# Performance work log

Measured on AMD Instinct MI355X. Metric: run time of the kernel, lower is better.

Reference implementation:

```python
import jax, jax.numpy as jnp
import numpy as np

# ---- module constants (from init_kwargs) ----
VOXEL_SIZE = np.array([0.1, 0.1, 0.2], np.float32)
PC_RANGE = np.array([0.0, -40.0, -3.0, 70.4, 40.0, 1.0], np.float32)
MAX_PTS = 10            # max_points_in_voxel
MAX_VOX = 40000         # max_voxel_num (hard voxelization cap per sample)
GRID = np.round((PC_RANGE[3:] - PC_RANGE[:3]) / VOXEL_SIZE).astype(np.int32)  # [704,800,20] (x,y,z)
BIG = int(GRID[0]) * int(GRID[1]) * int(GRID[2])

PC_MIN = jnp.asarray(PC_RANGE[:3])
VSIZE = jnp.asarray(VOXEL_SIZE)
GRID_J = jnp.asarray(GRID)

B = 8
N_PER_B = 120000


def setup_inputs() -> dict:
    key = jax.random.key(0)
    k1, = jax.random.split(key, 1)
    u = jax.random.uniform(k1, (B * N_PER_B, 4), dtype=jnp.float32)
    # place points inside (and slightly around) pc_range
    x = u[:, 0] * 72.0 - 0.5
    y = u[:, 1] * 82.0 - 41.0
    z = u[:, 2] * 4.4 - 3.2
    inten = u[:, 3]
    bs_idx = jnp.repeat(jnp.arange(B, dtype=jnp.float32), N_PER_B)
    points = jnp.stack([bs_idx, x, y, z, inten], axis=1)  # [960000, 5]
    return {"points": points, "batch_size": B}


def _voxelize_one(pts):
    """Hard voxelization of one point cloud pts [N,4] -> fixed-size buffers.
    Faithful to first-come voxel ordering and per-voxel point caps."""
    N = pts.shape[0]
    idxs = jnp.arange(N, dtype=jnp.int32)
    xyz = pts[:, :3]
    c = jnp.floor((xyz - PC_MIN) / VSIZE).astype(jnp.int32)  # [N,3] (x,y,z)
    valid = jnp.all((c >= 0) & (c < GRID_J), axis=1)
    lid = (c[:, 2] * GRID[1] + c[:, 1]) * GRID[0] + c[:, 0]  # z-major linear id
    lid = jnp.where(valid, lid, BIG)

    order = jnp.argsort(lid)            # stable: within a voxel, original order kept
    lid_s = lid[order]
    is_new = jnp.concatenate([jnp.ones((1,), bool), lid_s[1:] != lid_s[:-1]])
    gid = jnp.cumsum(is_new.astype(jnp.int32)) - 1           # group id per sorted point
    starts = jax.lax.cummax(jnp.where(is_new, idxs, 0))      # group start position
    pos = idxs - starts                                      # rank inside its voxel

    g_lid = jax.ops.segment_min(lid_s, gid, num_segments=N)
    g_valid = g_lid < BIG
    first_orig = jax.ops.segment_min(order.astype(jnp.int32), gid, num_segments=N)
    # voxel slot = first-appearance rank (invalid/empty groups pushed to the end)
    first_key = jnp.where(g_valid, first_orig, N + idxs)
    perm = jnp.argsort(first_key)
    slot = jnp.zeros(N, jnp.int32).at[perm].set(idxs)

    pslot = slot[gid]
    keep = g_valid[gid] & (pslot < MAX_VOX) & (pos < MAX_PTS)
    sslot = jnp.where(keep, pslot, MAX_VOX)   # overflow bucket, sliced off
    spos = jnp.where(keep, pos, 0)
    voxels = jnp.zeros((MAX_VOX + 1, MAX_PTS, pts.shape[1]), pts.dtype)
    voxels = voxels.at[sslot, spos].set(pts[order])[:MAX_VOX]

    gcount = jax.ops.segment_sum(keep.astype(jnp.int32), gid, num_segments=N)
    gslot = jnp.where(g_valid & (slot < MAX_VOX), slot, MAX_VOX)
    num_points = jnp.zeros(MAX_VOX + 1, jnp.int32).at[gslot].set(gcount)[:MAX_VOX]

    cs = c[order]
    gz = jax.ops.segment_min(cs[:, 2], gid, num_segments=N)
    gy = jax.ops.segment_min(cs[:, 1], gid, num_segments=N)
    gx = jax.ops.segment_min(cs[:, 0], gid, num_segments=N)
    coors = jnp.full((MAX_VOX + 1, 3), -1, jnp.int32)
    coors = coors.at[gslot].set(jnp.stack([gz, gy, gx], axis=1))[:MAX_VOX]  # (z,y,x)
    return voxels, num_points, coors


def reference(points, batch_size):
    feats = points[:, 1:]
    n_per_b = feats.shape[0] // batch_size  # points constructed contiguously per sample
    pts = feats.reshape(batch_size, n_per_b, feats.shape[1])
    voxels_b, num_b, coors_b = jax.vmap(_voxelize_one)(pts)
    voxels = voxels_b.reshape(batch_size * MAX_VOX, MAX_PTS, feats.shape[1])
    num_points = num_b.reshape(-1)
    batch_col = jnp.repeat(jnp.arange(batch_size, dtype=jnp.int32), MAX_VOX)[:, None]
    coors_batch = jnp.concatenate([batch_col, coors_b.reshape(-1, 3)], axis=1)  # [b,z,y,x]
    grid_size = jnp.asarray(GRID)
    return voxels, num_points, coors_batch, grid_size
```

## Files before the change

kernel.cpp:

```cpp
#include <hip/hip_runtime.h>

#define NB        8
#define NPB       120000
#define NPTS      (NB * NPB)
#define MAX_PTS   10
#define MAX_VOX   40000
#define GX        704
#define GY        800
#define GZ        20
#define CELLS     (GX * GY * GZ)

#define HC2       (1 << 18)
#define HMASK2    (HC2 - 1)
#define NSLOT2    (NB * HC2)

#define TILES     469
#define TILES_PAD 512
#define MBCAP     8192
#define MTILE     2048

#define EMPTY64   0xFFFFFFFFFFFFFFFFull

#define OUT_VOX   0LL
#define OUT_NUM   12800000LL
#define OUT_COOR  13120000LL
#define OUT_GRID  14400000LL

__device__ __forceinline__ bool point_cell(const float* __restrict__ p,
                                           int& cx, int& cy, int& cz) {
    cx = (int)floorf((p[1] - 0.0f)   / 0.1f);
    cy = (int)floorf((p[2] - (-40.0f)) / 0.1f);
    cz = (int)floorf((p[3] - (-3.0f))  / 0.2f);
    return (cx >= 0) & (cx < GX) & (cy >= 0) & (cy < GY) & (cz >= 0) & (cz < GZ);
}

__device__ __forceinline__ unsigned cell_hash(int lid) {
    return (((unsigned)lid * 2654435761u) >> 14) & HMASK2;
}

__global__ void k_init(float* __restrict__ out, ulonglong2* __restrict__ slab2,
                       unsigned* __restrict__ mcount) {
    int t = blockIdx.x * blockDim.x + threadIdx.x;
    int stride = gridDim.x * blockDim.x;
    ulonglong2 e2; e2.x = EMPTY64; e2.y = EMPTY64;
    for (int i = t; i < NSLOT2 / 2; i += stride) slab2[i] = e2;
    if (t < NB) mcount[t * 16] = 0u;
    if (t == 0) {
        out[OUT_GRID + 0] = 704.f;
        out[OUT_GRID + 1] = 800.f;
        out[OUT_GRID + 2] = 20.f;
    }
}

__global__ void k_insert(const float* __restrict__ pts,
                         unsigned long long* __restrict__ slabB,
                         int* __restrict__ lid32) {
    int b = blockIdx.x & 7;
    int idx = (blockIdx.x >> 3) * 256 + threadIdx.x;
    if (idx >= NPB) return;
    int g = b * NPB + idx;
    const float* p = pts + (long long)g * 5;
    int cx, cy, cz;
    if (!point_cell(p, cx, cy, cz)) { lid32[g] = -1; return; }
    int lid = (cz * GY + cy) * GX + cx;
    lid32[g] = lid;
    unsigned h = cell_hash(lid);
    unsigned long long key = ((unsigned long long)(unsigned)lid << 32)
                           | (unsigned long long)(unsigned)idx;
    unsigned long long* base = slabB + (size_t)b * HC2;
    while (true) {
        unsigned long long cur = *((volatile unsigned long long*)(base + h));
        if (cur == EMPTY64) {
            unsigned long long o = atomicCAS(base + h, EMPTY64, key);
            if (o == EMPTY64) break;
            cur = o;
        }
        if ((unsigned)(cur >> 32) == (unsigned)lid) {
            if ((unsigned)cur > (unsigned)idx) atomicMin(base + h, key);
            break;
        }
        h = (h + 1) & HMASK2;
    }
}

__global__ void k_rankscan(const int* __restrict__ lid32,
                           const unsigned long long* __restrict__ slabB,
                           unsigned char* __restrict__ rank8, int* __restrict__ tileSum) {
    int b = blockIdx.x & 7;
    int tile = blockIdx.x >> 3;
    int idx = tile * 256 + threadIdx.x;
    int f = 0;
    if (idx < NPB) {
        int lid = lid32[b * NPB + idx];
        if (lid >= 0) {
            const unsigned long long* base = slabB + (size_t)b * HC2;
            unsigned h = cell_hash(lid);
            unsigned long long cur;
            while (true) {
                cur = base[h];
                if ((unsigned)(cur >> 32) == (unsigned)lid) break;
                h = (h + 1) & HMASK2;
            }
            f = ((unsigned)cur == (unsigned)idx) ? 1 : 0;
        }
    }
    __shared__ int sc[256];
    sc[threadIdx.x] = f;
    __syncthreads();
    for (int off = 1; off < 256; off <<= 1) {
        int v = sc[threadIdx.x];
        if ((int)threadIdx.x >= off) v += sc[threadIdx.x - off];
        __syncthreads();
        sc[threadIdx.x] = v;
        __syncthreads();
    }
    if (idx < NPB) rank8[b * NPB + idx] = (unsigned char)(sc[threadIdx.x] - f);
    if (threadIdx.x == 255) tileSum[b * TILES_PAD + tile] = sc[255];
}

__global__ void k_finish(const float* __restrict__ pts, const int* __restrict__ lid32,
                         const unsigned char* __restrict__ rank8,
                         const int* __restrict__ tileSum,
                         const unsigned long long* __restrict__ slabB,
                         float* __restrict__ out, int2* __restrict__ mlist,
                         unsigned* __restrict__ mcount) {
    int b = blockIdx.x & 7;
    int tile = blockIdx.x >> 3;
    int t = threadIdx.x;

    __shared__ int sc[256];
    __shared__ int soff[TILES_PAD];
    int v0 = (2 * t     < TILES) ? tileSum[b * TILES_PAD + 2 * t]     : 0;
    int v1 = (2 * t + 1 < TILES) ? tileSum[b * TILES_PAD + 2 * t + 1] : 0;
    int w = v0 + v1;
    sc[t] = w;
    __syncthreads();
    for (int off = 1; off < 256; off <<= 1) {
        int x = sc[t];
        if (t >= off) x += sc[t - off];
        __syncthreads();
        sc[t] = x;
        __syncthreads();
    }
    int e = sc[t] - w;
    soff[2 * t] = e;
    soff[2 * t + 1] = e + v0;
    __syncthreads();

    int idx = tile * 256 + t;
    if (idx >= NPB) return;
    int g = b * NPB + idx;
    int lid = lid32[g];
    if (lid < 0) return;

    const unsigned long long* base = slabB + (size_t)b * HC2;
    unsigned h = cell_hash(lid);
    unsigned long long cur;
    while (true) {
        cur = base[h];
        if ((unsigned)(cur >> 32) == (unsigned)lid) break;
        h = (h + 1) & HMASK2;
    }
    unsigned minidx = (unsigned)cur;

    if (minidx == (unsigned)idx) {
        int slot = soff[idx >> 8] + (int)rank8[g];
        if (slot >= MAX_VOX) return;
        unsigned ul = (unsigned)lid;
        unsigned cx = ul % (unsigned)GX;
        unsigned tt = ul / (unsigned)GX;
        unsigned cy = tt % (unsigned)GY;
        unsigned cz = tt / (unsigned)GY;
        long long r = (long long)b * MAX_VOX + slot;
        ((float4*)(out + OUT_COOR))[r] = make_float4((float)b, (float)cz, (float)cy, (float)cx);
        out[OUT_NUM + r] = 1.f;
        const float* p = pts + (long long)g * 5;
        float4* row = (float4*)(out + OUT_VOX + r * (MAX_PTS * 4));
        row[0] = make_float4(p[1], p[2], p[3], p[4]);
        float4 zf = make_float4(0.f, 0.f, 0.f, 0.f);
        #pragma unroll
        for (int i = 1; i < MAX_PTS; i++) row[i] = zf;
    } else {
        int slot = soff[(int)minidx >> 8] + (int)rank8[b * NPB + (int)minidx];
        if (slot >= MAX_VOX) return;
        unsigned m = atomicAdd(&mcount[b * 16], 1u);
        if (m < MBCAP) mlist[(size_t)b * MBCAP + m] = make_int2(slot, idx);
    }
}

__global__ void k_multi(const float* __restrict__ pts,
                        const int2* __restrict__ mlist, const unsigned* __restrict__ mcount,
                        float* __restrict__ out) {
    int b = blockIdx.y;
    unsigned n = mcount[b * 16];
    if (n > MBCAP) n = MBCAP;
    unsigned t = blockIdx.x * blockDim.x + threadIdx.x;
    const int2* lst = mlist + (size_t)b * MBCAP;
    bool active = (t < n);
    int2 e = active ? lst[t] : make_int2(-1, -1);
    int pos = 1;
    int same = 0;
    __shared__ int2 sm[MTILE];
    for (unsigned chunk = 0; chunk < n; chunk += MTILE) {
        unsigned m = n - chunk;
        if (m > MTILE) m = MTILE;
        for (unsigned i = threadIdx.x; i < m; i += 256)
            sm[i] = lst[chunk + i];
        __syncthreads();
        if (active) {
            #pragma unroll 4
            for (unsigned j = 0; j < m; j++) {
                int2 o = sm[j];
                if (o.x == e.x) { same++; if (o.y < e.y) pos++; }
            }
        }
        __syncthreads();
    }
    if (!active) return;
    if (pos == 1) {
        int cnt = same + 1;
        out[OUT_NUM + (long long)b * MAX_VOX + e.x] =
            (float)(cnt < MAX_PTS ? cnt : MAX_PTS);
    }
    if (pos >= MAX_PTS) return;
    const float* p = pts + ((long long)b * NPB + e.y) * 5;
    ((float4*)(out + OUT_VOX))[(long long)(b * MAX_VOX + e.x) * MAX_PTS + pos] =
        make_float4(p[1], p[2], p[3], p[4]);
}

extern "C" void kernel_launch(void* const* d_in, const int* in_sizes, int n_in,
                              void* d_out, int out_size, void* d_ws, size_t ws_size,
                              hipStream_t stream) {
    const float* pts = (const float*)d_in[0];
    float* out = (float*)d_out;

    char* w = (char*)d_ws;
    unsigned long long* slabB = (unsigned long long*)w;
    w += (size_t)NSLOT2 * 8;
    unsigned char* rank8 = (unsigned char*)w; w += (size_t)NPTS;
    int* lid32 = (int*)w;    w += (size_t)NPTS * 4;
    int* tileSum = (int*)w;  w += (size_t)NB * TILES_PAD * 4;
    int2* mlist = (int2*)w;  w += (size_t)NB * MBCAP * 8;
    unsigned* mcount = (unsigned*)w; w += (size_t)NB * 16 * 4;

    const int PB = TILES * NB;
    k_init<<<dim3(2048), dim3(256), 0, stream>>>(out, (ulonglong2*)slabB, mcount);
    k_insert<<<dim3(PB), dim3(256), 0, stream>>>(pts, slabB, lid32);
    k_rankscan<<<dim3(PB), dim3(256), 0, stream>>>(lid32, slabB, rank8, tileSum);
    k_finish<<<dim3(PB), dim3(256), 0, stream>>>(pts, lid32, rank8, tileSum, slabB, out, mlist, mcount);
    k_multi<<<dim3(MBCAP / 256, NB), dim3(256), 0, stream>>>(pts, mlist, mcount, out);
}
```

Baseline: 185.5 us.

## Mark voxel-first points by scanning hash table instead of per-point probes

Adds a pass over the hash slab that sets a per-point flag for each voxel's first point, so rank-scan and finish read a byte instead of re-probing the hash table for every point; only non-first points still probe in finish. The insert loop also becomes a single atomicMin per step, which keeps the smaller key in place and carries the displaced larger key forward to the next probe slot. This trades redundant random hash probes for an extra kernel, a flag buffer that must be zeroed, and scattered byte writes.

```diff
diff --git a/kernel.cpp b/kernel.cpp
--- a/kernel.cpp
+++ b/kernel.cpp
@@ -39,11 +39,13 @@
 }
 
 __global__ void k_init(float* __restrict__ out, ulonglong2* __restrict__ slab2,
-                       unsigned* __restrict__ mcount) {
+                       uint4* __restrict__ flag4, unsigned* __restrict__ mcount) {
     int t = blockIdx.x * blockDim.x + threadIdx.x;
     int stride = gridDim.x * blockDim.x;
     ulonglong2 e2; e2.x = EMPTY64; e2.y = EMPTY64;
     for (int i = t; i < NSLOT2 / 2; i += stride) slab2[i] = e2;
+    uint4 z4 = make_uint4(0u, 0u, 0u, 0u);
+    for (int i = t; i < NPTS / 16; i += stride) flag4[i] = z4;
     if (t < NB) mcount[t * 16] = 0u;
     if (t == 0) {
         out[OUT_GRID + 0] = 704.f;
@@ -69,41 +71,30 @@
                            | (unsigned long long)(unsigned)idx;
     unsigned long long* base = slabB + (size_t)b * HC2;
     while (true) {
-        unsigned long long cur = *((volatile unsigned long long*)(base + h));
-        if (cur == EMPTY64) {
-            unsigned long long o = atomicCAS(base + h, EMPTY64, key);
-            if (o == EMPTY64) break;
-            cur = o;
-        }
-        if ((unsigned)(cur >> 32) == (unsigned)lid) {
-            if ((unsigned)cur > (unsigned)idx) atomicMin(base + h, key);
-            break;
-        }
+        unsigned long long old = atomicMin(base + h, key);
+        if (old == EMPTY64) break;
+        if ((old >> 32) == (key >> 32)) break;
+        if (old > key) key = old;
         h = (h + 1) & HMASK2;
     }
 }
 
-__global__ void k_rankscan(const int* __restrict__ lid32,
-                           const unsigned long long* __restrict__ slabB,
+__global__ void k_mark(const ulonglong2* __restrict__ slab2,
+                       unsigned char* __restrict__ flag) {
+    int b = blockIdx.x & 7;
+    int i = (blockIdx.x >> 3) * 256 + threadIdx.x;
+    ulonglong2 v = slab2[(size_t)b * (HC2 / 2) + i];
+    if (v.x != EMPTY64) flag[b * NPB + (unsigned)v.x] = 1;
+    if (v.y != EMPTY64) flag[b * NPB + (unsigned)v.y] = 1;
+}
+
+__global__ void k_rankscan(const unsigned char* __restrict__ flag,
                            unsigned char* __restrict__ rank8, int* __restrict__ tileSum) {
     int b = blockIdx.x & 7;
     int tile = blockIdx.x >> 3;
     int idx = tile * 256 + threadIdx.x;
     int f = 0;
-    if (idx < NPB) {
-        int lid = lid32[b * NPB + idx];
-        if (lid >= 0) {
-            const unsigned long long* base = slabB + (size_t)b * HC2;
-            unsigned h = cell_hash(lid);
-            unsigned long long cur;
-            while (true) {
-                cur = base[h];
-                if ((unsigned)(cur >> 32) == (unsigned)lid) break;
-                h = (h + 1) & HMASK2;
-            }
-            f = ((unsigned)cur == (unsigned)idx) ? 1 : 0;
-        }
-    }
+    if (idx < NPB) f = flag[b * NPB + idx];
     __shared__ int sc[256];
     sc[threadIdx.x] = f;
     __syncthreads();
@@ -119,6 +110,7 @@
 }
 
 __global__ void k_finish(const float* __restrict__ pts, const int* __restrict__ lid32,
+                         const unsigned char* __restrict__ flag,
                          const unsigned char* __restrict__ rank8,
                          const int* __restrict__ tileSum,
                          const unsigned long long* __restrict__ slabB,
@@ -153,17 +145,7 @@
     int lid = lid32[g];
     if (lid < 0) return;
 
-    const unsigned long long* base = slabB + (size_t)b * HC2;
-    unsigned h = cell_hash(lid);
-    unsigned long long cur;
-    while (true) {
-        cur = base[h];
-        if ((unsigned)(cur >> 32) == (unsigned)lid) break;
-        h = (h + 1) & HMASK2;
-    }
-    unsigned minidx = (unsigned)cur;
-
-    if (minidx == (unsigned)idx) {
+    if (flag[g]) {
         int slot = soff[idx >> 8] + (int)rank8[g];
         if (slot >= MAX_VOX) return;
         unsigned ul = (unsigned)lid;
@@ -181,6 +163,15 @@
         #pragma unroll
         for (int i = 1; i < MAX_PTS; i++) row[i] = zf;
     } else {
+        const unsigned long long* base = slabB + (size_t)b * HC2;
+        unsigned h = cell_hash(lid);
+        unsigned long long cur;
+        while (true) {
+            cur = base[h];
+            if ((unsigned)(cur >> 32) == (unsigned)lid) break;
+            h = (h + 1) & HMASK2;
+        }
+        unsigned minidx = (unsigned)cur;
         int slot = soff[(int)minidx >> 8] + (int)rank8[b * NPB + (int)minidx];
         if (slot >= MAX_VOX) return;
         unsigned m = atomicAdd(&mcount[b * 16], 1u);
@@ -237,6 +228,7 @@
     char* w = (char*)d_ws;
     unsigned long long* slabB = (unsigned long long*)w;
     w += (size_t)NSLOT2 * 8;
+    unsigned char* flag = (unsigned char*)w;  w += (size_t)NPTS;
     unsigned char* rank8 = (unsigned char*)w; w += (size_t)NPTS;
     int* lid32 = (int*)w;    w += (size_t)NPTS * 4;
     int* tileSum = (int*)w;  w += (size_t)NB * TILES_PAD * 4;
@@ -244,9 +236,10 @@
     unsigned* mcount = (unsigned*)w; w += (size_t)NB * 16 * 4;
 
     const int PB = TILES * NB;
-    k_init<<<dim3(2048), dim3(256), 0, stream>>>(out, (ulonglong2*)slabB, mcount);
+    k_init<<<dim3(2048), dim3(256), 0, stream>>>(out, (ulonglong2*)slabB, (uint4*)flag, mcount);
     k_insert<<<dim3(PB), dim3(256), 0, stream>>>(pts, slabB, lid32);
-    k_rankscan<<<dim3(PB), dim3(256), 0, stream>>>(lid32, slabB, rank8, tileSum);
-    k_finish<<<dim3(PB), dim3(256), 0, stream>>>(pts, lid32, rank8, tileSum, slabB, out, mlist, mcount);
+    k_mark<<<dim3(NB * (HC2 / 2 / 256)), dim3(256), 0, stream>>>((const ulonglong2*)slabB, flag);
+    k_rankscan<<<dim3(PB), dim3(256), 0, stream>>>(flag, rank8, tileSum);
+    k_finish<<<dim3(PB), dim3(256), 0, stream>>>(pts, lid32, flag, rank8, tileSum, slabB, out, mlist, mcount);
     k_multi<<<dim3(MBCAP / 256, NB), dim3(256), 0, stream>>>(pts, mlist, mcount, out);
 }
```

Measured after the change: 174.1 us. -6.2%, faster.
